# Kernel tuning notes

Measured on AMD Instinct MI355X. Metric: run time of the kernel, lower is better.

The kernel has to match this reference:

```python
import jax, jax.numpy as jnp
import numpy as np

CAPACITY = 0.125
AUX_W = 0.01
PRED_W = 0.01
N_HEADS = 16

def _bce_logits(x, t):
    # mean binary_cross_entropy_with_logits, numerically stable
    return jnp.mean(jnp.maximum(x, 0.0) - x * t + jnp.log1p(jnp.exp(-jnp.abs(x))))

def _rmsnorm(x, g, eps=1e-6):
    return x * jax.lax.rsqrt(jnp.mean(x * x, axis=-1, keepdims=True) + eps) * g

def _rope(x, pos):
    # x: [B,k,H,hd]; pos: [B,k] original token positions of selected tokens
    hd = x.shape[-1]
    inv = 1.0 / (10000.0 ** (jnp.arange(0, hd, 2, dtype=jnp.float32) / hd))
    ang = pos[..., None].astype(jnp.float32) * inv          # [B,k,hd/2]
    cos = jnp.cos(ang)[:, :, None, :]
    sin = jnp.sin(ang)[:, :, None, :]
    x1, x2 = jnp.split(x, 2, axis=-1)
    return jnp.concatenate([x1 * cos - x2 * sin, x2 * cos + x1 * sin], axis=-1)

def setup_inputs():
    key = jax.random.key(0)
    ks = jax.random.split(key, 16)
    B, T, D, F = 4, 4096, 1024, 4096
    s = 0.02
    w = lambda k, shape: (jax.random.normal(k, shape, jnp.float32) * s)
    return {
        'hidden_states': jax.random.normal(ks[0], (B, T, D), jnp.float32),
        'router_w': w(ks[1], (D,)),
        'fc1_w': w(ks[2], (D, D // 4)), 'fc1_b': jnp.zeros((D // 4,), jnp.float32),
        'fc2_w': w(ks[3], (D // 4,)), 'fc2_b': jnp.zeros((), jnp.float32),
        'ln1_g': jnp.ones((D,), jnp.float32), 'ln2_g': jnp.ones((D,), jnp.float32),
        'wq': w(ks[4], (D, D)), 'wk': w(ks[5], (D, D)),
        'wv': w(ks[6], (D, D)), 'wo': w(ks[7], (D, D)),
        'w_gate': w(ks[8], (D, F)), 'w_up': w(ks[9], (D, F)), 'w_down': w(ks[10], (F, D)),
        'training': 1,
    }

def reference(hidden_states, router_w, fc1_w, fc1_b, fc2_w, fc2_b, ln1_g, ln2_g,
              wq, wk, wv, wo, w_gate, w_up, w_down, training):
    B, T, D = hidden_states.shape
    H = N_HEADS
    hd = D // H
    k = max(1, int(T * CAPACITY))

    # ---- main router (training path) ----
    scores = hidden_states @ router_w                          # [B,T]
    _, topk_idx = jax.lax.top_k(scores, k)                     # [B,k]
    binary_targets = jnp.zeros_like(scores).at[
        jnp.arange(B)[:, None], topk_idx].set(1.0)
    main_aux = _bce_logits(scores, binary_targets) * AUX_W

    # ---- causal predictor on detached hidden states ----
    hs_det = jax.lax.stop_gradient(hidden_states)
    pred_logits = jax.nn.gelu(hs_det @ fc1_w + fc1_b) @ fc2_w + fc2_b  # [B,T]
    pred_loss = _bce_logits(pred_logits, jax.lax.stop_gradient(binary_targets))
    total_aux = main_aux + pred_loss * PRED_W

    # ---- select tokens (sorted to preserve causal order), gather ----
    idx = jnp.sort(topk_idx, axis=-1)                          # [B,k]
    gate = jax.nn.sigmoid(jnp.take_along_axis(scores, idx, axis=1))  # [B,k]
    sel = jnp.take_along_axis(hidden_states, idx[..., None], axis=1)  # [B,k,D]

    # ---- Qwen2-style decoder block on selected tokens ----
    a = _rmsnorm(sel, ln1_g)
    q = _rope((a @ wq).reshape(B, k, H, hd), idx)
    kk = _rope((a @ wk).reshape(B, k, H, hd), idx)
    v = (a @ wv).reshape(B, k, H, hd)
    att = jnp.einsum('bqhd,bkhd->bhqk', q, kk) / np.float32(np.sqrt(hd))
    causal = (idx[:, :, None] >= idx[:, None, :])[:, None, :, :]  # [B,1,k,k]
    att = jax.nn.softmax(jnp.where(causal, att, jnp.float32(-1e9)), axis=-1)
    attn_out = jnp.einsum('bhqk,bkhd->bqhd', att, v).reshape(B, k, D) @ wo
    h = sel + attn_out
    m = _rmsnorm(h, ln2_g)
    block_out = h + (jax.nn.silu(m @ w_gate) * (m @ w_up)) @ w_down   # [B,k,D]

    # ---- soft-gated scatter back into the residual stream ----
    upd = sel + gate[..., None] * (block_out - sel)
    new_states = hidden_states.at[jnp.arange(B)[:, None], idx].set(upd)
    return new_states, total_aux
```

## Files before the change

### kernel.cpp

```cpp
#include <hip/hip_runtime.h>
#include <math.h>

#define BB 4
#define TT 4096
#define DD 1024
#define FF 4096
#define NHH 16
#define HDD 64
#define KSEL 512
#define BT (BB*TT)
#define MTOK (BB*KSEL)
#define APAD 72

typedef __bf16 bf16x8 __attribute__((ext_vector_type(8)));
typedef __bf16 bf16x4 __attribute__((ext_vector_type(4)));
typedef float  f32x4  __attribute__((ext_vector_type(4)));

__device__ __forceinline__ void gl2lds16(const void* g, void* l) {
    __builtin_amdgcn_global_load_lds(
        (const __attribute__((address_space(1))) void*)g,
        (__attribute__((address_space(3))) void*)l,
        16, 0, 0);
}

__device__ __forceinline__ float gelu_tanh(float x) {
    return 0.5f * x * (1.0f + tanhf(0.7978845608028654f * (x + 0.044715f * x * x * x)));
}
__device__ __forceinline__ float bce_term(float x, float t) {
    return fmaxf(x, 0.f) - x * t + log1pf(expf(-fabsf(x)));
}

__global__ __launch_bounds__(256) void fused_pass(const float* __restrict__ hs,
                                                  const float* __restrict__ rw,
                                                  float* __restrict__ outp,
                                                  __bf16* __restrict__ hbf,
                                                  float* __restrict__ scores) {
    int wave = threadIdx.x >> 6, lane = threadIdx.x & 63;
    int row = blockIdx.x * 4 + wave;
    long base = (long)row * DD;
    float s = 0.f;
#pragma unroll
    for (int it = 0; it < 4; ++it) {
        int c = it * 256 + lane * 4;
        float4 v = *(const float4*)(hs + base + c);
        *(float4*)(outp + base + c) = v;
        float4 r4 = *(const float4*)(rw + c);
        s += v.x * r4.x + v.y * r4.y + v.z * r4.z + v.w * r4.w;
        bf16x4 b4 = {(__bf16)v.x, (__bf16)v.y, (__bf16)v.z, (__bf16)v.w};
        *(bf16x4*)(hbf + base + c) = b4;
    }
    for (int off = 32; off > 0; off >>= 1) s += __shfl_down(s, off, 64);
    if (lane == 0) scores[row] = s;
}

__global__ __launch_bounds__(1024) void topk_kernel(const float* __restrict__ scores,
                                                    float* __restrict__ flags,
                                                    int* __restrict__ idx_out,
                                                    float* __restrict__ gate_out) {
    int b = blockIdx.x;
    int tid = threadIdx.x;
    __shared__ float sv[TT];
    __shared__ int   si[TT];
    __shared__ int   tmp[KSEL];
    const float* sc = scores + b * TT;
    for (int i = tid; i < TT; i += 1024) { sv[i] = sc[i]; si[i] = i; }
    __syncthreads();
    for (int k2 = 2; k2 <= TT; k2 <<= 1) {
        for (int j = k2 >> 1; j > 0; j >>= 1) {
            for (int i = tid; i < TT; i += 1024) {
                int ixj = i ^ j;
                if (ixj > i) {
                    float s1 = sv[i], s2 = sv[ixj];
                    int i1 = si[i], i2 = si[ixj];
                    bool before = (s1 > s2) || (s1 == s2 && i1 < i2);
                    bool up = (i & k2) == 0;
                    if (up ? !before : before) {
                        sv[i] = s2; sv[ixj] = s1; si[i] = i2; si[ixj] = i1;
                    }
                }
            }
            __syncthreads();
        }
    }
    for (int i = tid; i < TT; i += 1024) flags[b * TT + i] = 0.f;
    __syncthreads();
    if (tid < KSEL) { tmp[tid] = si[tid]; flags[b * TT + si[tid]] = 1.0f; }
    __syncthreads();
    for (int k2 = 2; k2 <= KSEL; k2 <<= 1) {
        for (int j = k2 >> 1; j > 0; j >>= 1) {
            if (tid < KSEL) {
                int i = tid, ixj = tid ^ j;
                if (ixj > i) {
                    int a = tmp[i], c = tmp[ixj];
                    bool up = (i & k2) == 0;
                    if (up ? (a > c) : (a < c)) { tmp[i] = c; tmp[ixj] = a; }
                }
            }
            __syncthreads();
        }
    }
    if (tid < KSEL) {
        int t2 = tmp[tid];
        idx_out[b * KSEL + tid] = t2;
        float s = sc[t2];
        gate_out[b * KSEL + tid] = 1.0f / (1.0f + expf(-s));
    }
}

struct CDesc { const float* src; __bf16* dst; int K, N, start, ilv; };
struct CPack { CDesc d[5]; int nd; };

__global__ __launch_bounds__(256) void cast_multi(CPack p) {
    int bid = blockIdx.x, di = 0;
    while (di + 1 < p.nd && bid >= p.d[di + 1].start) ++di;
    const float* src = p.d[di].src;
    __bf16* dst = p.d[di].dst;
    int K = p.d[di].K, N = p.d[di].N, ilv = p.d[di].ilv;
    int local = bid - p.d[di].start;
    int tn = N >> 5;
    int n0 = (local % tn) * 32, k0 = (local / tn) * 32;
    __shared__ float tile[32][33];
    int tx = threadIdx.x & 31, ty = threadIdx.x >> 5;
#pragma unroll
    for (int i = 0; i < 32; i += 8)
        tile[ty + i][tx] = src[(long)(k0 + ty + i) * N + n0 + tx];
    __syncthreads();
#pragma unroll
    for (int i = 0; i < 32; i += 8) {
        int n = n0 + ty + i;
        int orow = n;
        if (ilv) orow = ((n >> 4) << 5) + (n & 15) + ((ilv == 2) ? 16 : 0);
        dst[(long)orow * K + k0 + tx] = (__bf16)tile[tx][ty + i];
    }
}

template <int EP>
__global__ __launch_bounds__(256) void mfma_gemm(const __bf16* __restrict__ Abf,
                                                 const __bf16* __restrict__ Bt,
                                                 int M, int N, int K,
                                                 __bf16* __restrict__ Cbf,
                                                 const float* __restrict__ hid,
                                                 const int* __restrict__ idxp,
                                                 const float* __restrict__ bias,
                                                 const float* __restrict__ w2,
                                                 float* __restrict__ logits) {
    __shared__ __bf16 As[128 * 32];
    __shared__ __bf16 Bs[128 * 32];
    int tid = threadIdx.x;
    int lane = tid & 63, wave = tid >> 6;
    int wm = wave >> 1, wn = wave & 1;
    int m0 = blockIdx.y * 128, n0 = blockIdx.x * 128;

    f32x4 zv = {0.f, 0.f, 0.f, 0.f};
    f32x4 acc[4][4];
#pragma unroll
    for (int i = 0; i < 4; ++i)
#pragma unroll
        for (int j = 0; j < 4; ++j) acc[i][j] = zv;

    int srow = tid >> 2;
    int scol = (tid & 3) * 8;
    long aoff = (long)(m0 + srow) * K + scol;
    long boff = (long)(n0 + srow) * K + scol;
    __bf16* ldsA = As + wave * 512;
    __bf16* ldsB = Bs + wave * 512;

    for (int k0 = 0; k0 < K; k0 += 32) {
        __syncthreads();
        gl2lds16(Abf + aoff + k0, ldsA);
        gl2lds16(Abf + aoff + (long)64 * K + k0, ldsA + 2048);
        gl2lds16(Bt + boff + k0, ldsB);
        gl2lds16(Bt + boff + (long)64 * K + k0, ldsB + 2048);
        __syncthreads();

        bf16x8 af[4], bfr[4];
#pragma unroll
        for (int mi = 0; mi < 4; ++mi)
            af[mi] = *(const bf16x8*)(As + (wm * 64 + mi * 16 + (lane & 15)) * 32 + (lane >> 4) * 8);
#pragma unroll
        for (int ni = 0; ni < 4; ++ni)
            bfr[ni] = *(const bf16x8*)(Bs + (wn * 64 + ni * 16 + (lane & 15)) * 32 + (lane >> 4) * 8);
#pragma unroll
        for (int mi = 0; mi < 4; ++mi)
#pragma unroll
            for (int ni = 0; ni < 4; ++ni)
                acc[mi][ni] = __builtin_amdgcn_mfma_f32_16x16x32_bf16(af[mi], bfr[ni], acc[mi][ni], 0, 0, 0);
    }

    int cm = (lane >> 4) * 4;
    int cn = lane & 15;
    if (EP == 3) {
#pragma unroll
        for (int mi = 0; mi < 4; ++mi) {
#pragma unroll
            for (int r = 0; r < 4; ++r) {
                float part = 0.f;
#pragma unroll
                for (int ni = 0; ni < 4; ++ni) {
                    int gn = n0 + wn * 64 + ni * 16 + cn;
                    float x = acc[mi][ni][r] + bias[gn];
                    part += gelu_tanh(x) * w2[gn];
                }
                part += __shfl_xor(part, 1, 64);
                part += __shfl_xor(part, 2, 64);
                part += __shfl_xor(part, 4, 64);
                part += __shfl_xor(part, 8, 64);
                if ((lane & 15) == 0)
                    atomicAdd(&logits[m0 + wm * 64 + mi * 16 + cm + r], part);
            }
        }
    } else if (EP == 1) {
#pragma unroll
        for (int mi = 0; mi < 4; ++mi)
#pragma unroll
            for (int ni = 0; ni < 4; ++ni)
#pragma unroll
                for (int r = 0; r < 4; ++r) {
                    int gm = m0 + wm * 64 + mi * 16 + cm + r;
                    int gn = n0 + wn * 64 + ni * 16 + cn;
                    int b = gm >> 9;
                    int row = idxp[gm];
                    float selv = hid[((long)b * TT + row) * DD + gn];
                    Cbf[(long)gm * N + gn] = (__bf16)(selv + acc[mi][ni][r]);
                }
    } else {
#pragma unroll
        for (int mi = 0; mi < 4; ++mi)
#pragma unroll
            for (int ni = 0; ni < 4; ++ni)
#pragma unroll
                for (int r = 0; r < 4; ++r) {
                    int gm = m0 + wm * 64 + mi * 16 + cm + r;
                    int gn = n0 + wn * 64 + ni * 16 + cn;
                    Cbf[(long)gm * N + gn] = (__bf16)acc[mi][ni][r];
                }
    }
}

__global__ __launch_bounds__(256) void gateup2_mfma(const __bf16* __restrict__ Abf,
                                                    const __bf16* __restrict__ Bt,
                                                    __bf16* __restrict__ act) {
    const int K = 1024;
    __shared__ __bf16 As[128 * 32];
    __shared__ __bf16 Bs[128 * 32];
    int tid = threadIdx.x;
    int lane = tid & 63, wave = tid >> 6;
    int wm = wave >> 1, wn = wave & 1;
    int m0 = blockIdx.y * 128, n0 = blockIdx.x * 128;

    f32x4 zv = {0.f, 0.f, 0.f, 0.f};
    f32x4 acc[4][4];
#pragma unroll
    for (int i = 0; i < 4; ++i)
#pragma unroll
        for (int j = 0; j < 4; ++j) acc[i][j] = zv;

    int srow = tid >> 2;
    int scol = (tid & 3) * 8;
    long aoff = (long)(m0 + srow) * K + scol;
    long boff = (long)(n0 + srow) * K + scol;
    __bf16* ldsA = As + wave * 512;
    __bf16* ldsB = Bs + wave * 512;

    for (int k0 = 0; k0 < K; k0 += 32) {
        __syncthreads();
        gl2lds16(Abf + aoff + k0, ldsA);
        gl2lds16(Abf + aoff + (long)64 * K + k0, ldsA + 2048);
        gl2lds16(Bt + boff + k0, ldsB);
        gl2lds16(Bt + boff + (long)64 * K + k0, ldsB + 2048);
        __syncthreads();

        bf16x8 af[4], bfr[4];
#pragma unroll
        for (int mi = 0; mi < 4; ++mi)
            af[mi] = *(const bf16x8*)(As + (wm * 64 + mi * 16 + (lane & 15)) * 32 + (lane >> 4) * 8);
#pragma unroll
        for (int ni = 0; ni < 4; ++ni)
            bfr[ni] = *(const bf16x8*)(Bs + (wn * 64 + ni * 16 + (lane & 15)) * 32 + (lane >> 4) * 8);
#pragma unroll
        for (int mi = 0; mi < 4; ++mi)
#pragma unroll
            for (int ni = 0; ni < 4; ++ni)
                acc[mi][ni] = __builtin_amdgcn_mfma_f32_16x16x32_bf16(af[mi], bfr[ni], acc[mi][ni], 0, 0, 0);
    }

    int cm = (lane >> 4) * 4;
    int cn = lane & 15;
    int colb = ((n0 + wn * 64) >> 1) + cn;
#pragma unroll
    for (int mi = 0; mi < 4; ++mi)
#pragma unroll
        for (int pi = 0; pi < 2; ++pi)
#pragma unroll
            for (int r = 0; r < 4; ++r) {
                int gm = m0 + wm * 64 + mi * 16 + cm + r;
                float g = acc[mi][2 * pi][r];
                float u = acc[mi][2 * pi + 1][r];
                float sl = g / (1.0f + expf(-g));
                act[(long)gm * 4096 + colb + pi * 16] = (__bf16)(sl * u);
            }
}

__global__ __launch_bounds__(256) void down_gemm(const __bf16* __restrict__ act,
                                                 const __bf16* __restrict__ Bt,
                                                 __bf16* __restrict__ p0,
                                                 __bf16* __restrict__ p1) {
    __shared__ __bf16 As[128 * 32];
    __shared__ __bf16 Bs[128 * 32];
    int tid = threadIdx.x;
    int lane = tid & 63, wave = tid >> 6;
    int wm = wave >> 1, wn = wave & 1;
    int m0 = blockIdx.y * 128, n0 = blockIdx.x * 128;
    int z = blockIdx.z;

    f32x4 zv = {0.f, 0.f, 0.f, 0.f};
    f32x4 acc[4][4];
#pragma unroll
    for (int i = 0; i < 4; ++i)
#pragma unroll
        for (int j = 0; j < 4; ++j) acc[i][j] = zv;

    int srow = tid >> 2;
    int scol = (tid & 3) * 8;
    long aoff = (long)(m0 + srow) * 4096 + z * 2048 + scol;
    long boff = (long)(n0 + srow) * 4096 + z * 2048 + scol;
    __bf16* ldsA = As + wave * 512;
    __bf16* ldsB = Bs + wave * 512;

    for (int k0 = 0; k0 < 2048; k0 += 32) {
        __syncthreads();
        gl2lds16(act + aoff + k0, ldsA);
        gl2lds16(act + aoff + (long)64 * 4096 + k0, ldsA + 2048);
        gl2lds16(Bt + boff + k0, ldsB);
        gl2lds16(Bt + boff + (long)64 * 4096 + k0, ldsB + 2048);
        __syncthreads();

        bf16x8 af[4], bfr[4];
#pragma unroll
        for (int mi = 0; mi < 4; ++mi)
            af[mi] = *(const bf16x8*)(As + (wm * 64 + mi * 16 + (lane & 15)) * 32 + (lane >> 4) * 8);
#pragma unroll
        for (int ni = 0; ni < 4; ++ni)
            bfr[ni] = *(const bf16x8*)(Bs + (wn * 64 + ni * 16 + (lane & 15)) * 32 + (lane >> 4) * 8);
#pragma unroll
        for (int mi = 0; mi < 4; ++mi)
#pragma unroll
            for (int ni = 0; ni < 4; ++ni)
                acc[mi][ni] = __builtin_amdgcn_mfma_f32_16x16x32_bf16(af[mi], bfr[ni], acc[mi][ni], 0, 0, 0);
    }

    int cm = (lane >> 4) * 4;
    int cn = lane & 15;
    __bf16* pz = z ? p1 : p0;
#pragma unroll
    for (int mi = 0; mi < 4; ++mi)
#pragma unroll
        for (int ni = 0; ni < 4; ++ni)
#pragma unroll
            for (int r = 0; r < 4; ++r) {
                int gm = m0 + wm * 64 + mi * 16 + cm + r;
                int gn = n0 + wn * 64 + ni * 16 + cn;
                pz[(long)gm * 1024 + gn] = (__bf16)acc[mi][ni][r];
            }
}

__global__ __launch_bounds__(256) void scatter_kernel(const __bf16* __restrict__ p0,
                                                      const __bf16* __restrict__ p1,
                                                      const __bf16* __restrict__ hbf,
                                                      const float* __restrict__ hid,
                                                      const int* __restrict__ idxp,
                                                      const float* __restrict__ gatep,
                                                      float* __restrict__ outp) {
    int m = blockIdx.x;
    int c = threadIdx.x * 4;
    int b = m >> 9;
    int row = idxp[m];
    float gv = gatep[m];
    long pb = (long)m * DD + c;
    bf16x4 v0 = *(const bf16x4*)(p0 + pb);
    bf16x4 v1 = *(const bf16x4*)(p1 + pb);
    bf16x4 hh = *(const bf16x4*)(hbf + pb);
    long ob = ((long)b * TT + row) * DD + c;
    float4 sel = *(const float4*)(hid + ob);
    float4 o;
    o.x = sel.x + gv * ((float)hh[0] + (float)v0[0] + (float)v1[0] - sel.x);
    o.y = sel.y + gv * ((float)hh[1] + (float)v0[1] + (float)v1[1] - sel.y);
    o.z = sel.z + gv * ((float)hh[2] + (float)v0[2] + (float)v1[2] - sel.z);
    o.w = sel.w + gv * ((float)hh[3] + (float)v0[3] + (float)v1[3] - sel.w);
    *(float4*)(outp + ob) = o;
}

template <typename TIN>
__global__ __launch_bounds__(256) void rms_kernel(const TIN* __restrict__ src,
                                                  const int* __restrict__ idx,
                                                  const float* __restrict__ gamma,
                                                  __bf16* __restrict__ out) {
    int m = blockIdx.x;
    int tid = threadIdx.x;
    long srow;
    if (idx) {
        int b = m >> 9;
        srow = ((long)b * TT + idx[m]) * DD;
    } else {
        srow = (long)m * DD;
    }
    __shared__ float red[256];
    float v[4];
#pragma unroll
    for (int i = 0; i < 4; ++i) v[i] = (float)src[srow + tid * 4 + i];
    float ss = v[0] * v[0] + v[1] * v[1] + v[2] * v[2] + v[3] * v[3];
    red[tid] = ss;
    __syncthreads();
    for (int s2 = 128; s2 > 0; s2 >>= 1) {
        if (tid < s2) red[tid] += red[tid + s2];
        __syncthreads();
    }
    float r = rsqrtf(red[0] / (float)DD + 1e-6f);
    float4 g4 = *(const float4*)(gamma + tid * 4);
    long obase = (long)m * DD + tid * 4;
    out[obase + 0] = (__bf16)(v[0] * r * g4.x);
    out[obase + 1] = (__bf16)(v[1] * r * g4.y);
    out[obase + 2] = (__bf16)(v[2] * r * g4.z);
    out[obase + 3] = (__bf16)(v[3] * r * g4.w);
}

__global__ __launch_bounds__(512) void rope_kernel(__bf16* __restrict__ qkv,
                                                   const int* __restrict__ idx) {
    int m = blockIdx.x;
    int t = threadIdx.x;
    int h = t >> 5, j = t & 31;
    float pos = (float)idx[m];
    float inv = expf(-((float)(2 * j) / (float)HDD) * 9.210340371976184f);
    float ang = pos * inv;
    float c = cosf(ang), s = sinf(ang);
    long base = (long)m * 3072 + h * HDD + j;
    float x1 = (float)qkv[base], x2 = (float)qkv[base + 32];
    qkv[base] = (__bf16)(x1 * c - x2 * s);
    qkv[base + 32] = (__bf16)(x2 * c + x1 * s);
    long kbase = base + 1024;
    x1 = (float)qkv[kbase]; x2 = (float)qkv[kbase + 32];
    qkv[kbase] = (__bf16)(x1 * c - x2 * s);
    qkv[kbase + 32] = (__bf16)(x2 * c + x1 * s);
}

__global__ __launch_bounds__(256) void attn_mfma(const __bf16* __restrict__ qkv,
                                                 __bf16* __restrict__ o) {
    int qt = blockIdx.x;
    int bh = blockIdx.y;
    int b = bh >> 4, h = bh & 15;
    int tid = threadIdx.x;
    int lane = tid & 63, w = tid >> 6;
    __shared__ __bf16 Ks[64 * APAD];
    __shared__ __bf16 Vt[64 * APAD];
    __shared__ __bf16 Ps[4][16 * APAD];

    int l15 = lane & 15, l4 = lane >> 4;
    int qrow0 = b * KSEL + qt * 64 + w * 16;
    bf16x8 qf[2];
    {
        long base = ((long)(qrow0 + l15)) * 3072 + h * 64 + l4 * 8;
        qf[0] = *(const bf16x8*)(qkv + base);
        qf[1] = *(const bf16x8*)(qkv + base + 32);
    }
    float m_run[4], l_run[4];
    f32x4 O[4];
#pragma unroll
    for (int r = 0; r < 4; ++r) { m_run[r] = -1e30f; l_run[r] = 0.f; }
    f32x4 zv = {0.f, 0.f, 0.f, 0.f};
#pragma unroll
    for (int ni = 0; ni < 4; ++ni) O[ni] = zv;

    int sr = tid & 63;
    int sg = tid >> 6;
    for (int kt = 0; kt <= qt; ++kt) {
        __syncthreads();
        long kvbase = ((long)(b * KSEL + kt * 64 + sr)) * 3072 + h * 64 + 1024;
        bf16x8 kv0 = *(const bf16x8*)(qkv + kvbase + sg * 16);
        bf16x8 kv1 = *(const bf16x8*)(qkv + kvbase + sg * 16 + 8);
        *(bf16x8*)(Ks + sr * APAD + sg * 16) = kv0;
        *(bf16x8*)(Ks + sr * APAD + sg * 16 + 8) = kv1;
        bf16x8 vv0 = *(const bf16x8*)(qkv + kvbase + 1024 + sg * 16);
        bf16x8 vv1 = *(const bf16x8*)(qkv + kvbase + 1024 + sg * 16 + 8);
#pragma unroll
        for (int i = 0; i < 8; ++i) {
            Vt[(sg * 16 + i) * APAD + sr] = vv0[i];
            Vt[(sg * 16 + 8 + i) * APAD + sr] = vv1[i];
        }
        __syncthreads();

        f32x4 S[4];
#pragma unroll
        for (int ni = 0; ni < 4; ++ni) S[ni] = zv;
#pragma unroll
        for (int ni = 0; ni < 4; ++ni) {
            bf16x8 kf0 = *(const bf16x8*)(Ks + (ni * 16 + l15) * APAD + l4 * 8);
            bf16x8 kf1 = *(const bf16x8*)(Ks + (ni * 16 + l15) * APAD + l4 * 8 + 32);
            S[ni] = __builtin_amdgcn_mfma_f32_16x16x32_bf16(qf[0], kf0, S[ni], 0, 0, 0);
            S[ni] = __builtin_amdgcn_mfma_f32_16x16x32_bf16(qf[1], kf1, S[ni], 0, 0, 0);
        }
        int rowb = qt * 64 + w * 16 + l4 * 4;
#pragma unroll
        for (int r = 0; r < 4; ++r) {
            float sv[4];
            float mx = -1e30f;
#pragma unroll
            for (int ni = 0; ni < 4; ++ni) {
                float x = S[ni][r] * 0.125f;
                int col = kt * 64 + ni * 16 + l15;
                if (col > rowb + r) x = -1e30f;
                sv[ni] = x;
                mx = fmaxf(mx, x);
            }
            mx = fmaxf(mx, __shfl_xor(mx, 1, 64));
            mx = fmaxf(mx, __shfl_xor(mx, 2, 64));
            mx = fmaxf(mx, __shfl_xor(mx, 4, 64));
            mx = fmaxf(mx, __shfl_xor(mx, 8, 64));
            float m_new = fmaxf(m_run[r], mx);
            float alpha = expf(m_run[r] - m_new);
            float ps = 0.f;
#pragma unroll
            for (int ni = 0; ni < 4; ++ni) {
                float e = expf(sv[ni] - m_new);
                sv[ni] = e;
                ps += e;
            }
            ps += __shfl_xor(ps, 1, 64);
            ps += __shfl_xor(ps, 2, 64);
            ps += __shfl_xor(ps, 4, 64);
            ps += __shfl_xor(ps, 8, 64);
            l_run[r] = l_run[r] * alpha + ps;
            m_run[r] = m_new;
#pragma unroll
            for (int ni = 0; ni < 4; ++ni) {
                O[ni][r] *= alpha;
                Ps[w][(l4 * 4 + r) * APAD + ni * 16 + l15] = (__bf16)sv[ni];
            }
        }
#pragma unroll
        for (int ks = 0; ks < 2; ++ks) {
            bf16x8 pf = *(const bf16x8*)(Ps[w] + l15 * APAD + ks * 32 + l4 * 8);
#pragma unroll
            for (int ni = 0; ni < 4; ++ni) {
                bf16x8 vf = *(const bf16x8*)(Vt + (ni * 16 + l15) * APAD + ks * 32 + l4 * 8);
                O[ni] = __builtin_amdgcn_mfma_f32_16x16x32_bf16(pf, vf, O[ni], 0, 0, 0);
            }
        }
    }
    long orow = (long)(b * KSEL + qt * 64 + w * 16);
#pragma unroll
    for (int r = 0; r < 4; ++r) {
        float inv = 1.0f / l_run[r];
#pragma unroll
        for (int ni = 0; ni < 4; ++ni)
            o[(orow + l4 * 4 + r) * DD + h * 64 + ni * 16 + l15] = (__bf16)(O[ni][r] * inv);
    }
}

__global__ __launch_bounds__(256) void bce_kernel(const float* __restrict__ scores,
                                                  const float* __restrict__ logits,
                                                  const float* __restrict__ flags,
                                                  const float* __restrict__ fc2b,
                                                  float* __restrict__ acc) {
    int i = blockIdx.x * 256 + threadIdx.x;
    int tid = threadIdx.x;
    __shared__ float r0[256];
    __shared__ float r1[256];
    float tgt = flags[i];
    r0[tid] = bce_term(scores[i], tgt);
    r1[tid] = bce_term(logits[i] + fc2b[0], tgt);
    __syncthreads();
    for (int s2 = 128; s2 > 0; s2 >>= 1) {
        if (tid < s2) { r0[tid] += r0[tid + s2]; r1[tid] += r1[tid + s2]; }
        __syncthreads();
    }
    if (tid == 0) {
        atomicAdd(acc + 0, r0[0]);
        atomicAdd(acc + 1, r1[0]);
    }
}

__global__ void finalize_kernel(const float* __restrict__ acc, float* __restrict__ out) {
    out[0] = (acc[0] / (float)BT) * 0.01f + (acc[1] / (float)BT) * 0.01f;
}

extern "C" void kernel_launch(void* const* d_in, const int* in_sizes, int n_in,
                              void* d_out, int out_size, void* d_ws, size_t ws_size,
                              hipStream_t stream) {
    const float* hidden = (const float*)d_in[0];
    const float* router_w = (const float*)d_in[1];
    const float* fc1_w = (const float*)d_in[2];
    const float* fc1_b = (const float*)d_in[3];
    const float* fc2_w = (const float*)d_in[4];
    const float* fc2_b = (const float*)d_in[5];
    const float* ln1_g = (const float*)d_in[6];
    const float* ln2_g = (const float*)d_in[7];
    const float* wq = (const float*)d_in[8];
    const float* wk = (const float*)d_in[9];
    const float* wv = (const float*)d_in[10];
    const float* wo = (const float*)d_in[11];
    const float* w_gate = (const float*)d_in[12];
    const float* w_up = (const float*)d_in[13];
    const float* w_down = (const float*)d_in[14];

    float* out = (float*)d_out;
    char* wsb = (char*)d_ws;

    float* scores = (float*)(wsb);
    float* flags  = (float*)(wsb + 0x10000);
    float* logits = (float*)(wsb + 0x20000);
    int*   idx    = (int*)  (wsb + 0x30000);
    float* gate   = (float*)(wsb + 0x32000);
    float* acc    = (float*)(wsb + 0x34000);
    __bf16* fc1_t  = (__bf16*)(wsb + 0x40000);
    __bf16* wo_t   = (__bf16*)(wsb + 0xC0000);
    __bf16* wqkv_t = (__bf16*)(wsb + 0x2C0000);
    __bf16* hidden_bf = (__bf16*)(wsb + 0x8C0000);
    __bf16* qkv    = (__bf16*)(wsb + 0x8C0000);
    __bf16* a_bf   = (__bf16*)(wsb + 0x14C0000);
    __bf16* act_bf = (__bf16*)(wsb + 0x8C0000);
    __bf16* att_bf = (__bf16*)(wsb + 0x18C0000);
    __bf16* h_bf   = (__bf16*)(wsb + 0x1CC0000);
    __bf16* m_bf   = (__bf16*)(wsb + 0x20C0000);
    __bf16* wgu_t  = (__bf16*)(wsb + 0x24C0000);
    __bf16* wd_t   = (__bf16*)(wsb + 0x24C0000);
    __bf16* p0     = (__bf16*)(wsb + 0x2CC0000);
    __bf16* p1     = (__bf16*)(wsb + 0x30C0000);

    hipMemsetAsync(acc, 0, 2 * sizeof(float), stream);
    hipMemsetAsync(logits, 0, BT * sizeof(float), stream);

    {
        CPack p;
        p.nd = 5;
        p.d[0] = {fc1_w, fc1_t, DD, 256, 0, 0};
        p.d[1] = {wq, wqkv_t, DD, DD, 256, 0};
        p.d[2] = {wk, wqkv_t + (size_t)1024 * 1024, DD, DD, 1280, 0};
        p.d[3] = {wv, wqkv_t + (size_t)2048 * 1024, DD, DD, 2304, 0};
        p.d[4] = {wo, wo_t, DD, DD, 3328, 0};
        cast_multi<<<4352, 256, 0, stream>>>(p);
    }

    fused_pass<<<BT / 4, 256, 0, stream>>>(hidden, router_w, out, hidden_bf, scores);
    topk_kernel<<<BB, 1024, 0, stream>>>(scores, flags, idx, gate);

    mfma_gemm<3><<<dim3(2, BT / 128), 256, 0, stream>>>(
        hidden_bf, fc1_t, BT, 256, DD, nullptr, nullptr, nullptr,
        fc1_b, fc2_w, logits);
    bce_kernel<<<BT / 256, 256, 0, stream>>>(scores, logits, flags, fc2_b, acc);

    rms_kernel<float><<<MTOK, 256, 0, stream>>>(hidden, idx, ln1_g, a_bf);

    mfma_gemm<0><<<dim3(3072 / 128, MTOK / 128), 256, 0, stream>>>(
        a_bf, wqkv_t, MTOK, 3072, DD, qkv, nullptr, nullptr,
        nullptr, nullptr, nullptr);
    rope_kernel<<<MTOK, 512, 0, stream>>>(qkv, idx);

    attn_mfma<<<dim3(KSEL / 64, BB * NHH), 256, 0, stream>>>(qkv, att_bf);

    {
        CPack p;
        p.nd = 2;
        p.d[0] = {w_gate, wgu_t, DD, FF, 0, 1};
        p.d[1] = {w_up,   wgu_t, DD, FF, 4096, 2};
        cast_multi<<<8192, 256, 0, stream>>>(p);
    }

    mfma_gemm<1><<<dim3(DD / 128, MTOK / 128), 256, 0, stream>>>(
        att_bf, wo_t, MTOK, DD, DD, h_bf, hidden, idx,
        nullptr, nullptr, nullptr);

    rms_kernel<__bf16><<<MTOK, 256, 0, stream>>>(h_bf, nullptr, ln2_g, m_bf);

    gateup2_mfma<<<dim3(8192 / 128, MTOK / 128), 256, 0, stream>>>(m_bf, wgu_t, act_bf);

    {
        CPack p;
        p.nd = 1;
        p.d[0] = {w_down, wd_t, FF, DD, 0, 0};
        cast_multi<<<4096, 256, 0, stream>>>(p);
    }

    down_gemm<<<dim3(DD / 128, MTOK / 128, 2), 256, 0, stream>>>(act_bf, wd_t, p0, p1);

    scatter_kernel<<<MTOK, 256, 0, stream>>>(p0, p1, h_bf, hidden, idx, gate, out);

    finalize_kernel<<<1, 1, 0, stream>>>(acc, out + (size_t)BT * DD);
}
```

Baseline: 524.5 us.

## Replace bitonic-sort top-k with two-pass radix select and prefix-sum compaction

The full bitonic sort of 4096 scores per batch, and the second sort of the selected indices, are replaced by a radix select. Two 12-bit histogram passes locate the threshold bucket, a small rank pass resolves ties in the final bucket, and a block prefix scan over selection flags writes the indices already in ascending order. This removes the many barrier-separated sort stages run by only four blocks. In exchange it relies on shared-memory atomics and a quadratic rank loop whose cost depends on how many scores fall into the last bucket.

```diff
diff --git a/kernel.cpp b/kernel.cpp
--- a/kernel.cpp
+++ b/kernel.cpp
@@ -53,58 +53,150 @@
     if (lane == 0) scores[row] = s;
 }
 
-__global__ __launch_bounds__(1024) void topk_kernel(const float* __restrict__ scores,
-                                                    float* __restrict__ flags,
-                                                    int* __restrict__ idx_out,
-                                                    float* __restrict__ gate_out) {
-    int b = blockIdx.x;
-    int tid = threadIdx.x;
-    __shared__ float sv[TT];
-    __shared__ int   si[TT];
-    __shared__ int   tmp[KSEL];
+__global__ __launch_bounds__(1024) void topk_radix(const float* __restrict__ scores,
+                                                   float* __restrict__ flags,
+                                                   int* __restrict__ idx_out,
+                                                   float* __restrict__ gate_out) {
+    int b = blockIdx.x, tid = threadIdx.x;
+    int lane = tid & 63, wid = tid >> 6;
+    __shared__ unsigned ku[TT];
+    __shared__ unsigned hist[4096];
+    __shared__ unsigned cand[4096];
+    __shared__ unsigned char selb[TT];
+    __shared__ unsigned wsum[16];
+    __shared__ int vars[8];
     const float* sc = scores + b * TT;
-    for (int i = tid; i < TT; i += 1024) { sv[i] = sc[i]; si[i] = i; }
-    __syncthreads();
-    for (int k2 = 2; k2 <= TT; k2 <<= 1) {
-        for (int j = k2 >> 1; j > 0; j >>= 1) {
-            for (int i = tid; i < TT; i += 1024) {
-                int ixj = i ^ j;
-                if (ixj > i) {
-                    float s1 = sv[i], s2 = sv[ixj];
-                    int i1 = si[i], i2 = si[ixj];
-                    bool before = (s1 > s2) || (s1 == s2 && i1 < i2);
-                    bool up = (i & k2) == 0;
-                    if (up ? !before : before) {
-                        sv[i] = s2; sv[ixj] = s1; si[i] = i2; si[ixj] = i1;
-                    }
-                }
+    const unsigned K = KSEL;
+
+    for (int i = tid; i < TT; i += 1024) {
+        unsigned u = __float_as_uint(sc[i]);
+        ku[i] = u ^ ((u & 0x80000000u) ? 0xFFFFFFFFu : 0x80000000u);
+    }
+    for (int j = tid; j < 4096; j += 1024) hist[j] = 0;
+    __syncthreads();
+    for (int i = tid; i < TT; i += 1024) atomicAdd(&hist[ku[i] >> 20], 1u);
+    __syncthreads();
+
+    unsigned c0 = hist[4 * tid], c1 = hist[4 * tid + 1];
+    unsigned c2 = hist[4 * tid + 2], c3 = hist[4 * tid + 3];
+    unsigned l3 = c3, l2 = c2 + l3, l1 = c1 + l2, l0 = c0 + l1;
+    unsigned v = l0;
+    for (int off = 1; off < 64; off <<= 1) {
+        unsigned o = (unsigned)__shfl_down((int)v, off, 64);
+        if (lane + off < 64) v += o;
+    }
+    if (lane == 0) wsum[wid] = v;
+    __syncthreads();
+    if (tid < 16) {
+        unsigned s = wsum[tid];
+        for (int off = 1; off < 16; off <<= 1) {
+            unsigned o = (unsigned)__shfl_down((int)s, off, 64);
+            if (tid + off < 16) s += o;
+        }
+        wsum[tid] = s;
+    }
+    __syncthreads();
+    unsigned wavetail = (wid + 1 < 16) ? wsum[wid + 1] : 0u;
+    unsigned tail = v + wavetail - l0;
+    unsigned S0 = l0 + tail, S1 = l1 + tail, S2 = l2 + tail, S3 = l3 + tail;
+    if (S0 >= K && S1 < K)   { vars[0] = 4 * tid;     vars[1] = (int)S1; }
+    if (S1 >= K && S2 < K)   { vars[0] = 4 * tid + 1; vars[1] = (int)S2; }
+    if (S2 >= K && S3 < K)   { vars[0] = 4 * tid + 2; vars[1] = (int)S3; }
+    if (S3 >= K && tail < K) { vars[0] = 4 * tid + 3; vars[1] = (int)tail; }
+    __syncthreads();
+    int B1 = vars[0];
+    unsigned need = K - (unsigned)vars[1];
+
+    for (int j = tid; j < 4096; j += 1024) hist[j] = 0;
+    __syncthreads();
+    for (int i = tid; i < TT; i += 1024)
+        if ((int)(ku[i] >> 20) == B1) atomicAdd(&hist[(ku[i] >> 8) & 0xFFFu], 1u);
+    __syncthreads();
+    c0 = hist[4 * tid]; c1 = hist[4 * tid + 1];
+    c2 = hist[4 * tid + 2]; c3 = hist[4 * tid + 3];
+    l3 = c3; l2 = c2 + l3; l1 = c1 + l2; l0 = c0 + l1;
+    v = l0;
+    for (int off = 1; off < 64; off <<= 1) {
+        unsigned o = (unsigned)__shfl_down((int)v, off, 64);
+        if (lane + off < 64) v += o;
+    }
+    if (lane == 0) wsum[wid] = v;
+    __syncthreads();
+    if (tid < 16) {
+        unsigned s = wsum[tid];
+        for (int off = 1; off < 16; off <<= 1) {
+            unsigned o = (unsigned)__shfl_down((int)s, off, 64);
+            if (tid + off < 16) s += o;
+        }
+        wsum[tid] = s;
+    }
+    if (tid == 0) vars[4] = 0;
+    __syncthreads();
+    wavetail = (wid + 1 < 16) ? wsum[wid + 1] : 0u;
+    tail = v + wavetail - l0;
+    S0 = l0 + tail; S1 = l1 + tail; S2 = l2 + tail; S3 = l3 + tail;
+    if (S0 >= need && S1 < need)   { vars[2] = 4 * tid;     vars[3] = (int)S1; }
+    if (S1 >= need && S2 < need)   { vars[2] = 4 * tid + 1; vars[3] = (int)S2; }
+    if (S2 >= need && S3 < need)   { vars[2] = 4 * tid + 2; vars[3] = (int)S3; }
+    if (S3 >= need && tail < need) { vars[2] = 4 * tid + 3; vars[3] = (int)tail; }
+    __syncthreads();
+    int B2 = vars[2];
+    unsigned need2 = need - (unsigned)vars[3];
+
+    for (int i = tid; i < TT; i += 1024) {
+        unsigned k = ku[i];
+        int top = (int)(k >> 20);
+        unsigned char s = 0;
+        if (top > B1) s = 1;
+        else if (top == B1) {
+            int sub = (int)((k >> 8) & 0xFFFu);
+            if (sub > B2) s = 1;
+            else if (sub == B2) {
+                unsigned pos = atomicAdd((unsigned*)&vars[4], 1u);
+                cand[pos] = ((k & 0xFFu) << 12) | (unsigned)(4095 - i);
             }
-            __syncthreads();
-        }
-    }
-    for (int i = tid; i < TT; i += 1024) flags[b * TT + i] = 0.f;
-    __syncthreads();
-    if (tid < KSEL) { tmp[tid] = si[tid]; flags[b * TT + si[tid]] = 1.0f; }
-    __syncthreads();
-    for (int k2 = 2; k2 <= KSEL; k2 <<= 1) {
-        for (int j = k2 >> 1; j > 0; j >>= 1) {
-            if (tid < KSEL) {
-                int i = tid, ixj = tid ^ j;
-                if (ixj > i) {
-                    int a = tmp[i], c = tmp[ixj];
-                    bool up = (i & k2) == 0;
-                    if (up ? (a > c) : (a < c)) { tmp[i] = c; tmp[ixj] = a; }
-                }
-            }
-            __syncthreads();
-        }
-    }
-    if (tid < KSEL) {
-        int t2 = tmp[tid];
-        idx_out[b * KSEL + tid] = t2;
-        float s = sc[t2];
-        gate_out[b * KSEL + tid] = 1.0f / (1.0f + expf(-s));
-    }
+        }
+        selb[i] = s;
+    }
+    __syncthreads();
+    int cn = vars[4];
+    for (int i = tid; i < cn; i += 1024) {
+        unsigned key = cand[i];
+        unsigned rank = 0;
+        for (int j = 0; j < cn; ++j) rank += (cand[j] > key) ? 1u : 0u;
+        if (rank < need2) selb[4095 - (int)(key & 0xFFFu)] = 1;
+    }
+    __syncthreads();
+
+    int i0 = 4 * tid;
+    int s0 = selb[i0], s1 = selb[i0 + 1], s2 = selb[i0 + 2], s3 = selb[i0 + 3];
+    flags[b * TT + i0]     = (float)s0;
+    flags[b * TT + i0 + 1] = (float)s1;
+    flags[b * TT + i0 + 2] = (float)s2;
+    flags[b * TT + i0 + 3] = (float)s3;
+    int totalv = s0 + s1 + s2 + s3;
+    unsigned pv = (unsigned)totalv;
+    for (int off = 1; off < 64; off <<= 1) {
+        unsigned o = (unsigned)__shfl_up((int)pv, off, 64);
+        if (lane >= off) pv += o;
+    }
+    if (lane == 63) wsum[wid] = pv;
+    __syncthreads();
+    if (tid < 16) {
+        unsigned s = wsum[tid];
+        for (int off = 1; off < 16; off <<= 1) {
+            unsigned o = (unsigned)__shfl_up((int)s, off, 64);
+            if (tid >= off) s += o;
+        }
+        wsum[tid] = s;
+    }
+    __syncthreads();
+    unsigned head = (wid > 0) ? wsum[wid - 1] : 0u;
+    int pos = (int)(pv + head) - totalv;
+    if (s0) { idx_out[b * KSEL + pos] = i0;     gate_out[b * KSEL + pos] = 1.f / (1.f + expf(-sc[i0]));     pos++; }
+    if (s1) { idx_out[b * KSEL + pos] = i0 + 1; gate_out[b * KSEL + pos] = 1.f / (1.f + expf(-sc[i0 + 1])); pos++; }
+    if (s2) { idx_out[b * KSEL + pos] = i0 + 2; gate_out[b * KSEL + pos] = 1.f / (1.f + expf(-sc[i0 + 2])); pos++; }
+    if (s3) { idx_out[b * KSEL + pos] = i0 + 3; gate_out[b * KSEL + pos] = 1.f / (1.f + expf(-sc[i0 + 3])); }
 }
 
 struct CDesc { const float* src; __bf16* dst; int K, N, start, ilv; };
@@ -641,7 +733,7 @@
     }
 
     fused_pass<<<BT / 4, 256, 0, stream>>>(hidden, router_w, out, hidden_bf, scores);
-    topk_kernel<<<BB, 1024, 0, stream>>>(scores, flags, idx, gate);
+    topk_radix<<<BB, 1024, 0, stream>>>(scores, flags, idx, gate);
 
     mfma_gemm<3><<<dim3(2, BT / 128), 256, 0, stream>>>(
         hidden_bf, fc1_t, BT, 256, DD, nullptr, nullptr, nullptr,
```

Measured after the change: 459.1 us. -12.5%, faster.
